# Kernel tuning notes

Measured on AMD Instinct MI355X. Metric: run time of the kernel, lower is better.

Reference implementation:

```python
import jax, jax.numpy as jnp
import numpy as np

L, D, H, DH, WS, FF = 4, 256, 8, 32, 128, 1024
B, N = 2, 8192
SCALE = DH ** -0.5
EPS = 1e-8


def setup_inputs() -> dict:
    key = jax.random.key(0)
    ks = jax.random.split(key, 24)
    nrm = lambda k, shape, s=0.02: jax.random.normal(k, shape, dtype=jnp.float32) * s
    d = {}
    d["x_real"] = jax.random.normal(ks[0], (B, N, D), dtype=jnp.float32)
    d["x_imag"] = jax.random.normal(ks[1], (B, N, D), dtype=jnp.float32)
    # complex attention projection weights, stored [in, out] (y = x @ W)
    d["Wq_r"] = nrm(ks[2], (L, D, D)); d["Wq_i"] = nrm(ks[3], (L, D, D))
    d["Wk_r"] = nrm(ks[4], (L, D, D)); d["Wk_i"] = nrm(ks[5], (L, D, D))
    d["Wv_r"] = nrm(ks[6], (L, D, D)); d["Wv_i"] = nrm(ks[7], (L, D, D))
    d["Wo_r"] = nrm(ks[8], (L, D, D)); d["Wo_i"] = nrm(ks[9], (L, D, D))
    d["rel_bias"] = nrm(ks[10], (L, 2 * WS + 1))  # std=0.02 per nn.init.normal_
    d["norm1_scale"] = jnp.ones((L, D), jnp.float32)
    d["norm2_scale"] = jnp.ones((L, D), jnp.float32)
    # ComplexFeedForward: real nn.Linear pairs with biases
    d["W1_r"] = nrm(ks[11], (L, D, FF)); d["b1_r"] = jnp.zeros((L, FF), jnp.float32)
    d["W1_i"] = nrm(ks[12], (L, D, FF)); d["b1_i"] = jnp.zeros((L, FF), jnp.float32)
    d["W2_r"] = nrm(ks[13], (L, FF, D)); d["b2_r"] = jnp.zeros((L, D), jnp.float32)
    d["W2_i"] = nrm(ks[14], (L, FF, D)); d["b2_i"] = jnp.zeros((L, D), jnp.float32)
    return d


def _rmsnorm(xr, xi, scale):
    rms = jnp.sqrt(jnp.mean(xr * xr + xi * xi, axis=-1, keepdims=True) + EPS)
    return xr / rms * scale, xi / rms * scale


def _cmm(xr, xi, Wr, Wi):
    # (xr + i xi) @ (Wr + i Wi)
    return xr @ Wr - xi @ Wi, xr @ Wi + xi @ Wr


def _split_heads(t):  # [B,N,H*DH] -> [B,H,NW,WS,DH]
    return t.reshape(B, N // WS, WS, H, DH).transpose(0, 3, 1, 2, 4)


def _attn(xr, xi, Wq_r, Wq_i, Wk_r, Wk_i, Wv_r, Wv_i, Wo_r, Wo_i, rel_bias):
    qr, qi = _cmm(xr, xi, Wq_r, Wq_i)
    kr, ki = _cmm(xr, xi, Wk_r, Wk_i)
    vr, vi = _cmm(xr, xi, Wv_r, Wv_i)
    qr, qi, kr, ki, vr, vi = map(_split_heads, (qr, qi, kr, ki, vr, vi))
    # Re(q . conj(k)) = qr.kr + qi.ki ; windowed (N % WS == 0, no padding)
    dots = (jnp.einsum('bhwid,bhwjd->bhwij', qr, kr)
            + jnp.einsum('bhwid,bhwjd->bhwij', qi, ki)) * SCALE
    idx = (jnp.arange(WS)[None, :] - jnp.arange(WS)[:, None]).clip(-WS, WS) + WS
    dots = dots + rel_bias[idx]  # broadcast over b,h,w
    attn = jax.nn.softmax(dots, axis=-1)  # real-valued probs
    or_ = jnp.einsum('bhwij,bhwjd->bhwid', attn, vr)
    oi_ = jnp.einsum('bhwij,bhwjd->bhwid', attn, vi)
    merge = lambda t: t.transpose(0, 2, 3, 1, 4).reshape(B, N, H * DH)
    or_, oi_ = merge(or_), merge(oi_)
    return _cmm(or_, oi_, Wo_r, Wo_i)


def _ffn(xr, xi, W1_r, b1_r, W1_i, b1_i, W2_r, b2_r, W2_i, b2_i):
    # faithful: w_real(x.real) - w_imag(x.imag) etc., each linear carries its bias
    hr = (xr @ W1_r + b1_r) - (xi @ W1_i + b1_i)
    hi = (xi @ W1_r + b1_r) + (xr @ W1_i + b1_i)
    hr = jax.nn.gelu(hr, approximate=False)
    hi = jax.nn.gelu(hi, approximate=False)
    yr = (hr @ W2_r + b2_r) - (hi @ W2_i + b2_i)
    yi = (hi @ W2_r + b2_r) + (hr @ W2_i + b2_i)
    return yr, yi


def _forward(x_real, x_imag, Wq_r, Wq_i, Wk_r, Wk_i, Wv_r, Wv_i, Wo_r, Wo_i,
             rel_bias, norm1_scale, norm2_scale,
             W1_r, b1_r, W1_i, b1_i, W2_r, b2_r, W2_i, b2_i):
    xr, xi = x_real, x_imag
    for l in range(L):
        nr, ni = _rmsnorm(xr, xi, norm1_scale[l])
        ar, ai = _attn(nr, ni, Wq_r[l], Wq_i[l], Wk_r[l], Wk_i[l],
                       Wv_r[l], Wv_i[l], Wo_r[l], Wo_i[l], rel_bias[l])
        xr, xi = xr + ar, xi + ai
        nr, ni = _rmsnorm(xr, xi, norm2_scale[l])
        fr, fi = _ffn(nr, ni, W1_r[l], b1_r[l], W1_i[l], b1_i[l],
                      W2_r[l], b2_r[l], W2_i[l], b2_i[l])
        xr, xi = xr + fr, xi + fi
    return jnp.stack([xr, xi])  # [2, B, N, D]


def reference(x_real, x_imag, Wq_r, Wq_i, Wk_r, Wk_i, Wv_r, Wv_i, Wo_r, Wo_i,
              rel_bias, norm1_scale, norm2_scale,
              W1_r, b1_r, W1_i, b1_i, W2_r, b2_r, W2_i, b2_i):
    return _forward(x_real, x_imag, Wq_r, Wq_i, Wk_r, Wk_i, Wv_r, Wv_i,
                    Wo_r, Wo_i, rel_bias, norm1_scale, norm2_scale,
                    W1_r, b1_r, W1_i, b1_i, W2_r, b2_r, W2_i, b2_i)
```

## Files before the change

kernel.cpp:

```cpp
#include <hip/hip_runtime.h>
#include <cstdint>


typedef __bf16 bf16x8 __attribute__((ext_vector_type(8)));
typedef float  f32x4  __attribute__((ext_vector_type(4)));

#define M_TOK 16384
#define PLANE 4194304

__device__ __forceinline__ unsigned short f2bf(float f) {
    union { float f; unsigned int u; } v; v.f = f;
    unsigned int r = v.u + 0x7FFFu + ((v.u >> 16) & 1u);
    return (unsigned short)(r >> 16);
}

__device__ __forceinline__ void async16(const void* g, void* l) {
    __builtin_amdgcn_global_load_lds(
        (const __attribute__((address_space(1))) void*)g,
        (__attribute__((address_space(3))) void*)l, 16, 0, 0);
}


__global__ __launch_bounds__(256) void copyin_kernel(const float* __restrict__ xr,
                                                     const float* __restrict__ xi,
                                                     float* __restrict__ X) {
    int idx = blockIdx.x * 256 + threadIdx.x;
    int p = idx >> 20;
    int rem = idx & 1048575;
    ((float4*)X)[idx] = p ? ((const float4*)xi)[rem] : ((const float4*)xr)[rem];
}


__global__ __launch_bounds__(256) void pack_qkv_kernel(
    const float* __restrict__ Wq_r, const float* __restrict__ Wq_i,
    const float* __restrict__ Wk_r, const float* __restrict__ Wk_i,
    const float* __restrict__ Wv_r, const float* __restrict__ Wv_i,
    unsigned short* __restrict__ out) {
    int idx = blockIdx.x * 256 + threadIdx.x;
    int l = idx / 786432;
    int rem = idx - l * 786432;
    int n = rem >> 9, k = rem & 511;
    int blk = n >> 8;
    int no = n & 255, kk = k & 255;
    bool khi = (k >= 256);
    bool imag = (blk & 1);
    const float *Wr, *Wi;
    int proj = blk >> 1;
    if (proj == 0)      { Wr = Wq_r; Wi = Wq_i; }
    else if (proj == 1) { Wr = Wk_r; Wi = Wk_i; }
    else                { Wr = Wv_r; Wi = Wv_i; }
    int wi = l * 65536 + kk * 256 + no;
    float val = !imag ? (khi ? -Wi[wi] : Wr[wi])
                      : (khi ?  Wr[wi] : Wi[wi]);
    out[idx] = f2bf(val);
}

__global__ __launch_bounds__(256) void pack_o_kernel(
    const float* __restrict__ Wo_r, const float* __restrict__ Wo_i,
    unsigned short* __restrict__ out) {
    int idx = blockIdx.x * 256 + threadIdx.x;
    int l = idx >> 18;
    int rem = idx & 262143;
    int n = rem >> 9, k = rem & 511;
    bool imag = (n >= 256);
    int no = n & 255, kk = k & 255;
    bool khi = (k >= 256);
    int wi = l * 65536 + kk * 256 + no;
    float val = !imag ? (khi ? -Wo_i[wi] : Wo_r[wi])
                      : (khi ?  Wo_r[wi] : Wo_i[wi]);
    out[idx] = f2bf(val);
}

__global__ __launch_bounds__(256) void pack_ffn1_kernel(
    const float* __restrict__ W1_r, const float* __restrict__ W1_i,
    unsigned short* __restrict__ out) {
    int idx = blockIdx.x * 256 + threadIdx.x;
    int l = idx >> 20;
    int rem = idx & 1048575;
    int n = rem >> 9, k = rem & 511;
    bool imag = (n >= 1024);
    int no = imag ? n - 1024 : n;
    int kk = k & 255;
    bool khi = (k >= 256);
    int wi = l * 262144 + kk * 1024 + no;
    float val = !imag ? (khi ? -W1_i[wi] : W1_r[wi])
                      : (khi ?  W1_r[wi] : W1_i[wi]);
    out[idx] = f2bf(val);
}

__global__ __launch_bounds__(256) void pack_ffn2_kernel(
    const float* __restrict__ W2_r, const float* __restrict__ W2_i,
    unsigned short* __restrict__ out) {
    int idx = blockIdx.x * 256 + threadIdx.x;
    int l = idx >> 20;
    int rem = idx & 1048575;
    int n = rem >> 11, k = rem & 2047;
    bool imag = (n >= 256);
    int no = n & 255;
    int kk = k & 1023;
    bool khi = (k >= 1024);
    int wi = l * 262144 + kk * 256 + no;
    float val = !imag ? (khi ? -W2_i[wi] : W2_r[wi])
                      : (khi ?  W2_r[wi] : W2_i[wi]);
    out[idx] = f2bf(val);
}

__global__ __launch_bounds__(256) void pack_bias_kernel(
    const float* __restrict__ b1r, const float* __restrict__ b1i,
    const float* __restrict__ b2r, const float* __restrict__ b2i,
    float* __restrict__ B1, float* __restrict__ B2) {
    int idx = blockIdx.x * 256 + threadIdx.x;
    if (idx < 8192) {
        int l = idx >> 11, n = idx & 2047;
        bool imag = (n >= 1024);
        int no = imag ? n - 1024 : n;
        int bi = l * 1024 + no;
        B1[idx] = imag ? (b1r[bi] + b1i[bi]) : (b1r[bi] - b1i[bi]);
    } else {
        int i2 = idx - 8192;
        int l = i2 >> 9, n = i2 & 511;
        bool imag = (n >= 256);
        int no = n & 255;
        int bi = l * 256 + no;
        B2[i2] = imag ? (b2r[bi] + b2i[bi]) : (b2r[bi] - b2i[bi]);
    }
}


__global__ __launch_bounds__(256) void rmsnorm_kernel(const float* __restrict__ X,
                                                      const float* __restrict__ scale,
                                                      unsigned short* __restrict__ out) {
    int row = blockIdx.x * 4 + (threadIdx.x >> 6);
    int lane = threadIdx.x & 63;
    float4 xr = ((const float4*)(X + (size_t)row * 256))[lane];
    float4 xi = ((const float4*)(X + PLANE + (size_t)row * 256))[lane];
    float ss = xr.x * xr.x + xr.y * xr.y + xr.z * xr.z + xr.w * xr.w
             + xi.x * xi.x + xi.y * xi.y + xi.z * xi.z + xi.w * xi.w;
#pragma unroll
    for (int m = 1; m < 64; m <<= 1) ss += __shfl_xor(ss, m);
    float inv = 1.0f / sqrtf(ss * (1.0f / 256.0f) + 1e-8f);
    float4 sc = ((const float4*)scale)[lane];
    ushort4 o0, o1;
    o0.x = f2bf(xr.x * inv * sc.x); o0.y = f2bf(xr.y * inv * sc.y);
    o0.z = f2bf(xr.z * inv * sc.z); o0.w = f2bf(xr.w * inv * sc.w);
    o1.x = f2bf(xi.x * inv * sc.x); o1.y = f2bf(xi.y * inv * sc.y);
    o1.z = f2bf(xi.z * inv * sc.z); o1.w = f2bf(xi.w * inv * sc.w);
    ushort4* orow = (ushort4*)(out + (size_t)row * 512);
    orow[lane] = o0;
    orow[64 + lane] = o1;
}


template <int K, int MODE>
__global__ __launch_bounds__(256, 2) void gemm4_kernel(
    const unsigned short* __restrict__ A, const unsigned short* __restrict__ Bt,
    unsigned short* __restrict__ Obf, const float* __restrict__ bias,
    float* __restrict__ Xres, int N, int nTn) {
    constexpr int NT = K >> 6;
    __shared__ __align__(16) char smem[65536];
    const int tid = threadIdx.x;
    const int lane = tid & 63;
    const int wave = tid >> 6;
    const int g = lane >> 4, rl = lane & 15;
    const int wm = wave >> 1, wn = wave & 1;

    const int nwg = gridDim.x;
    const int qs = nwg >> 3;
    const int wg = (blockIdx.x & 7) * qs + (blockIdx.x >> 3);
    const int tM = wg / nTn, tN = wg - tM * nTn;

    const unsigned short* pA[4];
    const unsigned short* pB[4];
    int dA[4], dB[4];
#pragma unroll
    for (int it = 0; it < 4; ++it) {
        int s = it * 256 + tid;
        int r = s >> 3, c = (s & 7) ^ (r & 7);
        pA[it] = A + (size_t)(tM * 128 + r) * K + c * 8;
        pB[it] = Bt + (size_t)(tN * 128 + r) * K + c * 8;
        dA[it] = (it * 256 + wave * 64) * 16;
        dB[it] = 16384 + (it * 256 + wave * 64) * 16;
    }
    int offA[2][4], offB[2][4];
#pragma unroll
    for (int ks = 0; ks < 2; ++ks) {
        int c = ks * 4 + g;
#pragma unroll
        for (int f = 0; f < 4; ++f) {
            int hrA = wm * 64 + f * 16 + rl;
            offA[ks][f] = hrA * 128 + ((c ^ (hrA & 7)) << 4);
            int hrB = wn * 64 + f * 16 + rl;
            offB[ks][f] = 16384 + hrB * 128 + ((c ^ (hrB & 7)) << 4);
        }
    }

    f32x4 acc[4][4];
#pragma unroll
    for (int i = 0; i < 4; ++i)
#pragma unroll
        for (int j = 0; j < 4; ++j)
#pragma unroll
            for (int v = 0; v < 4; ++v) acc[i][j][v] = 0.0f;

#pragma unroll
    for (int b = 0; b < 2; ++b) {
#pragma unroll
        for (int it = 0; it < 4; ++it) {
            async16(pA[it], smem + b * 32768 + dA[it]);
            async16(pB[it], smem + b * 32768 + dB[it]);
        }
#pragma unroll
        for (int it = 0; it < 4; ++it) { pA[it] += 64; pB[it] += 64; }
    }

#pragma unroll
    for (int t = 0; t < NT; ++t) {
        if (t + 1 < NT) asm volatile("s_waitcnt vmcnt(8)" ::: "memory");
        else            asm volatile("s_waitcnt vmcnt(0)" ::: "memory");
        __builtin_amdgcn_s_barrier();
        const int cur = (t & 1) * 32768;
#pragma unroll
        for (int ks = 0; ks < 2; ++ks) {
            bf16x8 aF[4], bF[4];
#pragma unroll
            for (int f = 0; f < 4; ++f) {
                aF[f] = *(const bf16x8*)(smem + cur + offA[ks][f]);
                bF[f] = *(const bf16x8*)(smem + cur + offB[ks][f]);
            }
#pragma unroll
            for (int fm = 0; fm < 4; ++fm)
#pragma unroll
                for (int fn = 0; fn < 4; ++fn)
                    acc[fm][fn] = __builtin_amdgcn_mfma_f32_16x16x32_bf16(
                        aF[fm], bF[fn], acc[fm][fn], 0, 0, 0);
        }
        __builtin_amdgcn_s_barrier();
        if (t + 2 < NT) {
#pragma unroll
            for (int it = 0; it < 4; ++it) {
                async16(pA[it], smem + cur + dA[it]);
                async16(pB[it], smem + cur + dB[it]);
            }
#pragma unroll
            for (int it = 0; it < 4; ++it) { pA[it] += 64; pB[it] += 64; }
        }
    }

#pragma unroll
    for (int fm = 0; fm < 4; ++fm)
#pragma unroll
        for (int fn = 0; fn < 4; ++fn)
#pragma unroll
            for (int v = 0; v < 4; ++v) {
                int row = tM * 128 + wm * 64 + fm * 16 + g * 4 + v;
                int col = tN * 128 + wn * 64 + fn * 16 + rl;
                float val = acc[fm][fn][v];
                if (MODE == 0) {
                    Obf[(size_t)row * N + col] = f2bf(val);
                } else if (MODE == 1) {
                    float x = val + bias[col];
                    float ge = 0.5f * x * (1.0f + erff(x * 0.70710678118654752f));
                    Obf[(size_t)row * N + col] = f2bf(ge);
                } else {
                    float x = val + (bias ? bias[col] : 0.0f);
                    size_t off = (col < 256 ? 0 : (size_t)PLANE)
                               + (size_t)row * 256 + (col & 255);
                    Xres[off] += x;
                }
            }
}


#define AT_KOFF 16384
#define AT_VOFF 34816
#define AT_ROFF 52224

__global__ __launch_bounds__(256) void attn_kernel(
    const unsigned short* __restrict__ qkv, const float* __restrict__ relb_g,
    unsigned short* __restrict__ attout) {
    __shared__ __align__(16) char smem[53264];
    const int tid = threadIdx.x;
    const int lane = tid & 63;
    const int wq = tid >> 6;
    const int g = lane >> 4;
    const int rl = lane & 15;
    const int w = blockIdx.x, h = blockIdx.y, b = blockIdx.z;
    const int tok0 = b * 8192 + w * 128;
    float* relb = (float*)(smem + AT_ROFF);

    for (int i = tid; i < 257; i += 256) relb[i] = relb_g[i];

#pragma unroll
    for (int it = 0; it < 4; ++it) {
        int s = it * 256 + tid;
        int r = s >> 3;
        int c = (s & 7) ^ (r & 7);
        int colq = (c < 4) ? (h * 32 + c * 8) : (256 + h * 32 + (c - 4) * 8);
        const unsigned short* rowp = qkv + (size_t)(tok0 + r) * 1536;
        *(float4*)(smem + s * 16) = *(const float4*)(rowp + colq);
        *(float4*)(smem + AT_KOFF + s * 16) = *(const float4*)(rowp + colq + 512);
    }
#pragma unroll
    for (int it = 0; it < 4; ++it) {
        int e = it * 256 + tid;
        int j = e >> 3;
        int d0 = (e & 7) * 8;
        int colv = (d0 < 32) ? (1024 + h * 32 + d0) : (1280 + h * 32 + (d0 - 32));
        float4 vv = *(const float4*)(qkv + (size_t)(tok0 + j) * 1536 + colv);
        const unsigned short* u = (const unsigned short*)&vv;
#pragma unroll
        for (int k = 0; k < 8; ++k)
            *(unsigned short*)(smem + AT_VOFF + ((d0 + k) * 136 + j) * 2) = u[k];
    }
    __syncthreads();

    f32x4 accS[2][8];
#pragma unroll
    for (int i = 0; i < 2; ++i)
#pragma unroll
        for (int j = 0; j < 8; ++j)
#pragma unroll
            for (int v = 0; v < 4; ++v) accS[i][j][v] = 0.0f;

#pragma unroll
    for (int ks = 0; ks < 2; ++ks) {
        bf16x8 qf[2], kf[8];
        int c = ks * 4 + g;
#pragma unroll
        for (int fm = 0; fm < 2; ++fm) {
            int r = wq * 32 + fm * 16 + rl;
            qf[fm] = *(const bf16x8*)(smem + r * 128 + ((c ^ (r & 7)) << 4));
        }
#pragma unroll
        for (int fn = 0; fn < 8; ++fn) {
            int r = fn * 16 + rl;
            kf[fn] = *(const bf16x8*)(smem + AT_KOFF + r * 128 + ((c ^ (r & 7)) << 4));
        }
#pragma unroll
        for (int fm = 0; fm < 2; ++fm)
#pragma unroll
            for (int fn = 0; fn < 8; ++fn)
                accS[fm][fn] = __builtin_amdgcn_mfma_f32_16x16x32_bf16(
                    qf[fm], kf[fn], accS[fm][fn], 0, 0, 0);
    }

#pragma unroll
    for (int fm = 0; fm < 2; ++fm)
#pragma unroll
        for (int v = 0; v < 4; ++v) {
            int i = wq * 32 + fm * 16 + g * 4 + v;
            float m = -1e30f;
#pragma unroll
            for (int fn = 0; fn < 8; ++fn) {
                int j = fn * 16 + rl;
                float s = accS[fm][fn][v] * 0.17677669529663687f + relb[j - i + 128];
                accS[fm][fn][v] = s;
                m = fmaxf(m, s);
            }
            m = fmaxf(m, __shfl_xor(m, 1));
            m = fmaxf(m, __shfl_xor(m, 2));
            m = fmaxf(m, __shfl_xor(m, 4));
            m = fmaxf(m, __shfl_xor(m, 8));
            float sum = 0.0f;
#pragma unroll
            for (int fn = 0; fn < 8; ++fn) {
                float p = __expf(accS[fm][fn][v] - m);
                accS[fm][fn][v] = p;
                sum += p;
            }
            sum += __shfl_xor(sum, 1);
            sum += __shfl_xor(sum, 2);
            sum += __shfl_xor(sum, 4);
            sum += __shfl_xor(sum, 8);
            float inv = 1.0f / sum;
#pragma unroll
            for (int fn = 0; fn < 8; ++fn) accS[fm][fn][v] *= inv;
        }

    __syncthreads();

#pragma unroll
    for (int fm = 0; fm < 2; ++fm)
#pragma unroll
        for (int fn = 0; fn < 8; ++fn)
#pragma unroll
            for (int v = 0; v < 4; ++v) {
                int i = wq * 32 + fm * 16 + g * 4 + v;
                int j = fn * 16 + rl;
                ((unsigned short*)smem)[i * 136 + j] = f2bf(accS[fm][fn][v]);
            }
    __syncthreads();

    f32x4 accO[2][4];
#pragma unroll
    for (int i = 0; i < 2; ++i)
#pragma unroll
        for (int j = 0; j < 4; ++j)
#pragma unroll
            for (int v = 0; v < 4; ++v) accO[i][j][v] = 0.0f;

#pragma unroll
    for (int ks = 0; ks < 4; ++ks) {
        bf16x8 pf[2], vf[4];
#pragma unroll
        for (int fm = 0; fm < 2; ++fm) {
            int r = wq * 32 + fm * 16 + rl;
            pf[fm] = *(const bf16x8*)(smem + r * 272 + ks * 64 + g * 16);
        }
#pragma unroll
        for (int fn = 0; fn < 4; ++fn) {
            int n = fn * 16 + rl;
            vf[fn] = *(const bf16x8*)(smem + AT_VOFF + n * 272 + ks * 64 + g * 16);
        }
#pragma unroll
        for (int fm = 0; fm < 2; ++fm)
#pragma unroll
            for (int fn = 0; fn < 4; ++fn)
                accO[fm][fn] = __builtin_amdgcn_mfma_f32_16x16x32_bf16(
                    pf[fm], vf[fn], accO[fm][fn], 0, 0, 0);
    }

#pragma unroll
    for (int fm = 0; fm < 2; ++fm)
#pragma unroll
        for (int fn = 0; fn < 4; ++fn)
#pragma unroll
            for (int v = 0; v < 4; ++v) {
                int i = wq * 32 + fm * 16 + g * 4 + v;
                int dc = fn * 16 + rl;
                int col = (dc < 32) ? (h * 32 + dc) : (256 + h * 32 + (dc - 32));
                attout[(size_t)(tok0 + i) * 512 + col] = f2bf(accO[fm][fn][v]);
            }
}


extern "C" void kernel_launch(void* const* d_in, const int* in_sizes, int n_in,
                              void* d_out, int out_size, void* d_ws, size_t ws_size,
                              hipStream_t stream) {
    const float* x_real = (const float*)d_in[0];
    const float* x_imag = (const float*)d_in[1];
    const float* Wq_r = (const float*)d_in[2];
    const float* Wq_i = (const float*)d_in[3];
    const float* Wk_r = (const float*)d_in[4];
    const float* Wk_i = (const float*)d_in[5];
    const float* Wv_r = (const float*)d_in[6];
    const float* Wv_i = (const float*)d_in[7];
    const float* Wo_r = (const float*)d_in[8];
    const float* Wo_i = (const float*)d_in[9];
    const float* rel_bias = (const float*)d_in[10];
    const float* norm1 = (const float*)d_in[11];
    const float* norm2 = (const float*)d_in[12];
    const float* W1_r = (const float*)d_in[13];
    const float* b1_r = (const float*)d_in[14];
    const float* W1_i = (const float*)d_in[15];
    const float* b1_i = (const float*)d_in[16];
    const float* W2_r = (const float*)d_in[17];
    const float* b2_r = (const float*)d_in[18];
    const float* W2_i = (const float*)d_in[19];
    const float* b2_i = (const float*)d_in[20];

    float* X = (float*)d_out;

    char* ws = (char*)d_ws;
    unsigned short* NRM  = (unsigned short*)(ws + 0);
    unsigned short* QKVH = (unsigned short*)(ws + 16777216);
    unsigned short* ATTO = (unsigned short*)(ws + 83886080);
    unsigned short* WQKV = (unsigned short*)(ws + 100663296);
    unsigned short* WO   = (unsigned short*)(ws + 106954752);
    unsigned short* W1P  = (unsigned short*)(ws + 109051904);
    unsigned short* W2P  = (unsigned short*)(ws + 117440512);
    float*          B1   = (float*)(ws + 125829120);
    float*          B2   = (float*)(ws + 125861888);

    copyin_kernel<<<8192, 256, 0, stream>>>(x_real, x_imag, X);
    pack_qkv_kernel<<<12288, 256, 0, stream>>>(Wq_r, Wq_i, Wk_r, Wk_i, Wv_r, Wv_i, WQKV);
    pack_o_kernel<<<4096, 256, 0, stream>>>(Wo_r, Wo_i, WO);
    pack_ffn1_kernel<<<16384, 256, 0, stream>>>(W1_r, W1_i, W1P);
    pack_ffn2_kernel<<<16384, 256, 0, stream>>>(W2_r, W2_i, W2P);
    pack_bias_kernel<<<40, 256, 0, stream>>>(b1_r, b1_i, b2_r, b2_i, B1, B2);

    for (int l = 0; l < 4; ++l) {
        rmsnorm_kernel<<<4096, 256, 0, stream>>>(X, norm1 + l * 256, NRM);
        gemm4_kernel<512, 0><<<1536, 256, 0, stream>>>(
            NRM, WQKV + (size_t)l * 786432, QKVH, nullptr, nullptr, 1536, 12);
        attn_kernel<<<dim3(64, 8, 2), 256, 0, stream>>>(QKVH, rel_bias + l * 257, ATTO);
        gemm4_kernel<512, 2><<<512, 256, 0, stream>>>(
            ATTO, WO + (size_t)l * 262144, nullptr, nullptr, X, 512, 4);
        rmsnorm_kernel<<<4096, 256, 0, stream>>>(X, norm2 + l * 256, NRM);
        gemm4_kernel<512, 1><<<2048, 256, 0, stream>>>(
            NRM, W1P + (size_t)l * 1048576, QKVH, B1 + l * 2048, nullptr, 2048, 16);
        gemm4_kernel<2048, 2><<<512, 256, 0, stream>>>(
            QKVH, W2P + (size_t)l * 1048576, nullptr, B2 + l * 512, X, 512, 4);
    }
}
```

Before: 983.0 us.

## Load GEMM B fragments directly to registers and stage only A through LDS

The GEMM kernel no longer stages the B (weight) tile through LDS with async global-to-LDS loads. Each wave now loads its B MFMA fragments straight from global memory into a double-buffered register set. The A tile is prefetched into registers and written into a halved, double-buffered LDS region with the XOR swizzle. This halves LDS use and LDS traffic for B, at the cost of more registers, duplicated B global loads across the two wm waves, and register-staged rather than async copies for A.

```diff
diff --git a/kernel.cpp b/kernel.cpp
--- a/kernel.cpp
+++ b/kernel.cpp
@@ -12,12 +12,6 @@
     union { float f; unsigned int u; } v; v.f = f;
     unsigned int r = v.u + 0x7FFFu + ((v.u >> 16) & 1u);
     return (unsigned short)(r >> 16);
-}
-
-__device__ __forceinline__ void async16(const void* g, void* l) {
-    __builtin_amdgcn_global_load_lds(
-        (const __attribute__((address_space(1))) void*)g,
-        (__attribute__((address_space(3))) void*)l, 16, 0, 0);
 }
 
 
@@ -152,12 +146,12 @@
 
 
 template <int K, int MODE>
-__global__ __launch_bounds__(256, 2) void gemm4_kernel(
+__global__ __launch_bounds__(256, 2) void gemm5_kernel(
     const unsigned short* __restrict__ A, const unsigned short* __restrict__ Bt,
     unsigned short* __restrict__ Obf, const float* __restrict__ bias,
     float* __restrict__ Xres, int N, int nTn) {
     constexpr int NT = K >> 6;
-    __shared__ __align__(16) char smem[65536];
+    __shared__ __align__(16) char smem[32768];
     const int tid = threadIdx.x;
     const int lane = tid & 63;
     const int wave = tid >> 6;
@@ -170,27 +164,32 @@
     const int tM = wg / nTn, tN = wg - tM * nTn;
 
     const unsigned short* pA[4];
-    const unsigned short* pB[4];
-    int dA[4], dB[4];
+    int dsW[4];
 #pragma unroll
     for (int it = 0; it < 4; ++it) {
         int s = it * 256 + tid;
-        int r = s >> 3, c = (s & 7) ^ (r & 7);
+        int r = s >> 3, c = s & 7;
         pA[it] = A + (size_t)(tM * 128 + r) * K + c * 8;
-        pB[it] = Bt + (size_t)(tN * 128 + r) * K + c * 8;
-        dA[it] = (it * 256 + wave * 64) * 16;
-        dB[it] = 16384 + (it * 256 + wave * 64) * 16;
-    }
-    int offA[2][4], offB[2][4];
+        dsW[it] = r * 128 + ((c ^ (r & 7)) << 4);
+    }
+    int offA[2][4];
 #pragma unroll
     for (int ks = 0; ks < 2; ++ks) {
         int c = ks * 4 + g;
 #pragma unroll
         for (int f = 0; f < 4; ++f) {
-            int hrA = wm * 64 + f * 16 + rl;
-            offA[ks][f] = hrA * 128 + ((c ^ (hrA & 7)) << 4);
-            int hrB = wn * 64 + f * 16 + rl;
-            offB[ks][f] = 16384 + hrB * 128 + ((c ^ (hrB & 7)) << 4);
+            int hr = wm * 64 + f * 16 + rl;
+            offA[ks][f] = hr * 128 + ((c ^ (hr & 7)) << 4);
+        }
+    }
+    const unsigned short* pB[2][4];
+#pragma unroll
+    for (int ks = 0; ks < 2; ++ks) {
+        int c = ks * 4 + g;
+#pragma unroll
+        for (int fn = 0; fn < 4; ++fn) {
+            int row = tN * 128 + wn * 64 + fn * 16 + rl;
+            pB[ks][fn] = Bt + (size_t)row * K + c * 8;
         }
     }
 
@@ -202,48 +201,51 @@
 #pragma unroll
             for (int v = 0; v < 4; ++v) acc[i][j][v] = 0.0f;
 
-#pragma unroll
-    for (int b = 0; b < 2; ++b) {
-#pragma unroll
-        for (int it = 0; it < 4; ++it) {
-            async16(pA[it], smem + b * 32768 + dA[it]);
-            async16(pB[it], smem + b * 32768 + dB[it]);
-        }
-#pragma unroll
-        for (int it = 0; it < 4; ++it) { pA[it] += 64; pB[it] += 64; }
-    }
+    uint4 aR[4];
+    bf16x8 bR[2][2][4];
+
+#pragma unroll
+    for (int it = 0; it < 4; ++it) { aR[it] = *(const uint4*)pA[it]; pA[it] += 64; }
+#pragma unroll
+    for (int ks = 0; ks < 2; ++ks)
+#pragma unroll
+        for (int fn = 0; fn < 4; ++fn) { bR[0][ks][fn] = *(const bf16x8*)pB[ks][fn]; pB[ks][fn] += 64; }
+#pragma unroll
+    for (int it = 0; it < 4; ++it) *(uint4*)(smem + dsW[it]) = aR[it];
+    __syncthreads();
 
 #pragma unroll
     for (int t = 0; t < NT; ++t) {
-        if (t + 1 < NT) asm volatile("s_waitcnt vmcnt(8)" ::: "memory");
-        else            asm volatile("s_waitcnt vmcnt(0)" ::: "memory");
-        __builtin_amdgcn_s_barrier();
-        const int cur = (t & 1) * 32768;
+        if (t + 1 < NT) {
+#pragma unroll
+            for (int it = 0; it < 4; ++it) { aR[it] = *(const uint4*)pA[it]; pA[it] += 64; }
+#pragma unroll
+            for (int ks = 0; ks < 2; ++ks)
+#pragma unroll
+                for (int fn = 0; fn < 4; ++fn) {
+                    bR[(t + 1) & 1][ks][fn] = *(const bf16x8*)pB[ks][fn];
+                    pB[ks][fn] += 64;
+                }
+        }
 #pragma unroll
         for (int ks = 0; ks < 2; ++ks) {
-            bf16x8 aF[4], bF[4];
-#pragma unroll
-            for (int f = 0; f < 4; ++f) {
-                aF[f] = *(const bf16x8*)(smem + cur + offA[ks][f]);
-                bF[f] = *(const bf16x8*)(smem + cur + offB[ks][f]);
-            }
+            bf16x8 aF[4];
+#pragma unroll
+            for (int f = 0; f < 4; ++f)
+                aF[f] = *(const bf16x8*)(smem + (t & 1) * 16384 + offA[ks][f]);
 #pragma unroll
             for (int fm = 0; fm < 4; ++fm)
 #pragma unroll
                 for (int fn = 0; fn < 4; ++fn)
                     acc[fm][fn] = __builtin_amdgcn_mfma_f32_16x16x32_bf16(
-                        aF[fm], bF[fn], acc[fm][fn], 0, 0, 0);
-        }
-        __builtin_amdgcn_s_barrier();
-        if (t + 2 < NT) {
-#pragma unroll
-            for (int it = 0; it < 4; ++it) {
-                async16(pA[it], smem + cur + dA[it]);
-                async16(pB[it], smem + cur + dB[it]);
-            }
-#pragma unroll
-            for (int it = 0; it < 4; ++it) { pA[it] += 64; pB[it] += 64; }
-        }
+                        aF[fm], bR[t & 1][ks][fn], acc[fm][fn], 0, 0, 0);
+        }
+        if (t + 1 < NT) {
+#pragma unroll
+            for (int it = 0; it < 4; ++it)
+                *(uint4*)(smem + ((t + 1) & 1) * 16384 + dsW[it]) = aR[it];
+        }
+        __syncthreads();
     }
 
 #pragma unroll
@@ -481,15 +483,15 @@
 
     for (int l = 0; l < 4; ++l) {
         rmsnorm_kernel<<<4096, 256, 0, stream>>>(X, norm1 + l * 256, NRM);
-        gemm4_kernel<512, 0><<<1536, 256, 0, stream>>>(
+        gemm5_kernel<512, 0><<<1536, 256, 0, stream>>>(
             NRM, WQKV + (size_t)l * 786432, QKVH, nullptr, nullptr, 1536, 12);
         attn_kernel<<<dim3(64, 8, 2), 256, 0, stream>>>(QKVH, rel_bias + l * 257, ATTO);
-        gemm4_kernel<512, 2><<<512, 256, 0, stream>>>(
+        gemm5_kernel<512, 2><<<512, 256, 0, stream>>>(
             ATTO, WO + (size_t)l * 262144, nullptr, nullptr, X, 512, 4);
         rmsnorm_kernel<<<4096, 256, 0, stream>>>(X, norm2 + l * 256, NRM);
-        gemm4_kernel<512, 1><<<2048, 256, 0, stream>>>(
+        gemm5_kernel<512, 1><<<2048, 256, 0, stream>>>(
             NRM, W1P + (size_t)l * 1048576, QKVH, B1 + l * 2048, nullptr, 2048, 16);
-        gemm4_kernel<2048, 2><<<512, 256, 0, stream>>>(
+        gemm5_kernel<2048, 2><<<512, 256, 0, stream>>>(
             QKVH, W2P + (size_t)l * 1048576, nullptr, B2 + l * 512, X, 512, 4);
     }
 }
```

New measurement: 1.396 ms. +42.0%, slower.

## Add 256x256-tile 8-wave ping-pong GEMM kernel for QKV and FFN projections

Applied to the files above, without the earlier changes.

Introduces gemm8_kernel: 512 threads, a 256x256 output tile, 128KB double-buffered LDS in half-tile stages, and an interleaved schedule of async global-to-LDS loads, LDS fragment reads and MFMA bursts raised in priority with s_setprio. It also remaps block IDs so consecutive tiles are spread across the XCD groups. The QKV, FFN1 and FFN2 GEMMs switch to it, with grids shrunk to match. The larger tile aims for more reuse per loaded byte and better MFMA density. In exchange, occupancy drops to one block per CU given the LDS size, and FFN2 launches only 128 blocks, which may leave many CUs idle.

```diff
diff --git a/kernel.cpp b/kernel.cpp
--- a/kernel.cpp
+++ b/kernel.cpp
@@ -255,6 +255,169 @@
                 int row = tM * 128 + wm * 64 + fm * 16 + g * 4 + v;
                 int col = tN * 128 + wn * 64 + fn * 16 + rl;
                 float val = acc[fm][fn][v];
+                if (MODE == 0) {
+                    Obf[(size_t)row * N + col] = f2bf(val);
+                } else if (MODE == 1) {
+                    float x = val + bias[col];
+                    float ge = 0.5f * x * (1.0f + erff(x * 0.70710678118654752f));
+                    Obf[(size_t)row * N + col] = f2bf(ge);
+                } else {
+                    float x = val + (bias ? bias[col] : 0.0f);
+                    size_t off = (col < 256 ? 0 : (size_t)PLANE)
+                               + (size_t)row * 256 + (col & 255);
+                    Xres[off] += x;
+                }
+            }
+}
+
+
+template <int K, int MODE>
+__global__ __launch_bounds__(512, 2) void gemm8_kernel(
+    const unsigned short* __restrict__ A, const unsigned short* __restrict__ Bt,
+    unsigned short* __restrict__ Obf, const float* __restrict__ bias,
+    float* __restrict__ Xres, int N, int nTn) {
+    constexpr int NT = K >> 6;
+    constexpr int NIT = NT >> 1;
+    constexpr int NTM = NT - 1;
+    __shared__ __align__(16) char smem[131072];
+    const int tid = threadIdx.x, lane = tid & 63, wave = tid >> 6;
+    const int g = lane >> 4, rl = lane & 15;
+    const int wm = wave >> 2, wn = wave & 3;
+
+    const int nwg = gridDim.x, qs = nwg >> 3;
+    const int wg = (blockIdx.x & 7) * qs + (blockIdx.x >> 3);
+    const int tM = wg / nTn, tN = wg - tM * nTn;
+
+    const unsigned short* sA[2];
+    const unsigned short* sB[2];
+    int ldsOff[2];
+#pragma unroll
+    for (int it = 0; it < 2; ++it) {
+        int s = it * 512 + tid;
+        int r = s >> 3, cch = (s & 7) ^ (r & 7);
+        sA[it] = A + (size_t)(tM * 256 + r) * K + cch * 8;
+        sB[it] = Bt + (size_t)(tN * 256 + r) * K + cch * 8;
+        ldsOff[it] = (it * 512 + wave * 64) * 16;
+    }
+    auto stageA = [&](int tt, int h, int buf) {
+        int t = tt & NTM;
+        char* base = smem + ((buf * 2 + h) << 14);
+#pragma unroll
+        for (int it = 0; it < 2; ++it)
+            async16(sA[it] + (size_t)h * 128 * K + t * 64, base + ldsOff[it]);
+    };
+    auto stageB = [&](int tt, int h, int buf) {
+        int t = tt & NTM;
+        char* base = smem + 65536 + ((buf * 2 + h) << 14);
+#pragma unroll
+        for (int it = 0; it < 2; ++it)
+            async16(sB[it] + (size_t)h * 128 * K + t * 64, base + ldsOff[it]);
+    };
+
+    int rdA[4][2], rdB[2][2];
+#pragma unroll
+    for (int fm = 0; fm < 4; ++fm)
+#pragma unroll
+        for (int ks = 0; ks < 2; ++ks) {
+            int r = fm * 16 + rl, c = ks * 4 + g;
+            rdA[fm][ks] = r * 128 + ((c ^ (r & 7)) << 4);
+        }
+#pragma unroll
+    for (int fn = 0; fn < 2; ++fn)
+#pragma unroll
+        for (int ks = 0; ks < 2; ++ks) {
+            int r = (wn & 1) * 64 + fn * 16 + rl, c = ks * 4 + g;
+            rdB[fn][ks] = r * 128 + ((c ^ (r & 7)) << 4);
+        }
+    char* aBase[2];
+    char* bBase[2];
+    aBase[0] = smem + (wm << 14);            aBase[1] = smem + ((2 + wm) << 14);
+    bBase[0] = smem + 65536 + ((wn >> 1) << 14); bBase[1] = smem + 65536 + ((2 + (wn >> 1)) << 14);
+
+    f32x4 acc[8][4];
+#pragma unroll
+    for (int i = 0; i < 8; ++i)
+#pragma unroll
+        for (int j = 0; j < 4; ++j)
+#pragma unroll
+            for (int v = 0; v < 4; ++v) acc[i][j][v] = 0.0f;
+
+    bf16x8 aF[4][2], bF0[2][2], bF1[2][2];
+
+#define LOADA(BUF, QM)                                                         \
+    {                                                                          \
+        char* hb = aBase[BUF] + (QM) * 8192;                                   \
+        _Pragma("unroll") for (int fm = 0; fm < 4; ++fm)                       \
+            _Pragma("unroll") for (int ks = 0; ks < 2; ++ks)                   \
+                aF[fm][ks] = *(const bf16x8*)(hb + rdA[fm][ks]);               \
+    }
+#define LOADB(BUF, QN, DST)                                                    \
+    {                                                                          \
+        char* hb = bBase[BUF] + (QN) * 4096;                                   \
+        _Pragma("unroll") for (int fn = 0; fn < 2; ++fn)                       \
+            _Pragma("unroll") for (int ks = 0; ks < 2; ++ks)                   \
+                DST[fn][ks] = *(const bf16x8*)(hb + rdB[fn][ks]);              \
+    }
+#define MFMA16(QM, QN, BF)                                                     \
+    __builtin_amdgcn_s_setprio(1);                                             \
+    _Pragma("unroll") for (int fm = 0; fm < 4; ++fm)                           \
+        _Pragma("unroll") for (int fn = 0; fn < 2; ++fn)                       \
+            _Pragma("unroll") for (int ks = 0; ks < 2; ++ks)                   \
+                acc[(QM)*4 + fm][(QN)*2 + fn] =                                \
+                    __builtin_amdgcn_mfma_f32_16x16x32_bf16(                   \
+                        aF[fm][ks], BF[fn][ks], acc[(QM)*4 + fm][(QN)*2 + fn], \
+                        0, 0, 0);                                              \
+    __builtin_amdgcn_s_setprio(0);
+#define BAR() __builtin_amdgcn_s_barrier()
+#define LGKM0() asm volatile("s_waitcnt lgkmcnt(0)" ::: "memory")
+#define VM4() asm volatile("s_waitcnt vmcnt(4)" ::: "memory")
+
+    stageB(0, 0, 0); stageA(0, 0, 0); stageB(0, 1, 0); stageA(0, 1, 0);
+    stageB(1, 0, 1); stageA(1, 0, 1);
+    VM4();
+    BAR();
+
+    for (int i = 0; i < NIT; ++i) {
+        const int t0 = 2 * i;
+        LOADA(0, 0); LOADB(0, 0, bF0);
+        stageB(t0 + 1, 1, 1);
+        BAR(); LGKM0(); MFMA16(0, 0, bF0); BAR();
+        LOADB(0, 1, bF1);
+        stageA(t0 + 1, 1, 1);
+        BAR(); LGKM0(); MFMA16(0, 1, bF1); BAR();
+        LOADA(0, 1);
+        stageB(t0 + 2, 0, 0);
+        BAR(); LGKM0(); MFMA16(1, 1, bF1); BAR();
+        stageA(t0 + 2, 0, 0);
+        BAR(); LGKM0(); MFMA16(1, 0, bF0); VM4(); BAR();
+        LOADA(1, 0); LOADB(1, 0, bF0);
+        stageB(t0 + 2, 1, 0);
+        BAR(); LGKM0(); MFMA16(0, 0, bF0); BAR();
+        LOADB(1, 1, bF1);
+        stageA(t0 + 2, 1, 0);
+        BAR(); LGKM0(); MFMA16(0, 1, bF1); BAR();
+        LOADA(1, 1);
+        stageB(t0 + 3, 0, 1);
+        BAR(); LGKM0(); MFMA16(1, 1, bF1); BAR();
+        stageA(t0 + 3, 0, 1);
+        BAR(); LGKM0(); MFMA16(1, 0, bF0); VM4(); BAR();
+    }
+#undef LOADA
+#undef LOADB
+#undef MFMA16
+#undef BAR
+#undef LGKM0
+#undef VM4
+
+#pragma unroll
+    for (int i8 = 0; i8 < 8; ++i8)
+#pragma unroll
+        for (int j4 = 0; j4 < 4; ++j4)
+#pragma unroll
+            for (int v = 0; v < 4; ++v) {
+                int row = tM * 256 + wm * 128 + (i8 >> 2) * 64 + (i8 & 3) * 16 + g * 4 + v;
+                int col = tN * 256 + wn * 64 + (j4 >> 1) * 32 + (j4 & 1) * 16 + rl;
+                float val = acc[i8][j4][v];
                 if (MODE == 0) {
                     Obf[(size_t)row * N + col] = f2bf(val);
                 } else if (MODE == 1) {
@@ -481,15 +644,15 @@
 
     for (int l = 0; l < 4; ++l) {
         rmsnorm_kernel<<<4096, 256, 0, stream>>>(X, norm1 + l * 256, NRM);
-        gemm4_kernel<512, 0><<<1536, 256, 0, stream>>>(
-            NRM, WQKV + (size_t)l * 786432, QKVH, nullptr, nullptr, 1536, 12);
+        gemm8_kernel<512, 0><<<384, 512, 0, stream>>>(
+            NRM, WQKV + (size_t)l * 786432, QKVH, nullptr, nullptr, 1536, 6);
         attn_kernel<<<dim3(64, 8, 2), 256, 0, stream>>>(QKVH, rel_bias + l * 257, ATTO);
         gemm4_kernel<512, 2><<<512, 256, 0, stream>>>(
             ATTO, WO + (size_t)l * 262144, nullptr, nullptr, X, 512, 4);
         rmsnorm_kernel<<<4096, 256, 0, stream>>>(X, norm2 + l * 256, NRM);
-        gemm4_kernel<512, 1><<<2048, 256, 0, stream>>>(
-            NRM, W1P + (size_t)l * 1048576, QKVH, B1 + l * 2048, nullptr, 2048, 16);
-        gemm4_kernel<2048, 2><<<512, 256, 0, stream>>>(
-            QKVH, W2P + (size_t)l * 1048576, nullptr, B2 + l * 512, X, 512, 4);
-    }
-}
+        gemm8_kernel<512, 1><<<512, 512, 0, stream>>>(
+            NRM, W1P + (size_t)l * 1048576, QKVH, B1 + l * 2048, nullptr, 2048, 8);
+        gemm8_kernel<2048, 2><<<128, 512, 0, stream>>>(
+            QKVH, W2P + (size_t)l * 1048576, nullptr, B2 + l * 512, X, 512, 2);
+    }
+}
```

Result: slower. 1.177 ms (+19.7%).
